# Kernel optimization log

Hardware: AMD Instinct MI355X
Metric: run time of the kernel (lower is better)

## Reference

```python
import jax, jax.numpy as jnp
import numpy as np

B, C, H, W = 16, 512, 64, 64
CB, CG = 64, 256  # bottleneck = C/8, g = C/2


def _conv1x1(x, w, b):
    # x: [B,Cin,H,W], w: [Cout,Cin] -> [B,Cout,H,W]
    return jnp.einsum('bchw,oc->bohw', x, w) + b[None, :, None, None]


def _avg_pool2(x):
    # 2x2 average pool, stride 2. x: [B,C,H,W] with even H,W.
    b, c, h, w = x.shape
    return x.reshape(b, c, h // 2, 2, w // 2, 2).mean(axis=(3, 5))


def setup_inputs() -> dict:
    key = jax.random.key(0)
    ks = jax.random.split(key, 6)
    s = 0.02
    return {
        'x': jax.random.normal(ks[0], (B, C, H, W), jnp.float32),
        'w_theta': jax.random.normal(ks[1], (CB, C), jnp.float32) * s,
        'b_theta': jnp.zeros((CB,), jnp.float32),
        'w_phi': jax.random.normal(ks[2], (CB, C), jnp.float32) * s,
        'b_phi': jnp.zeros((CB,), jnp.float32),
        'w_g': jax.random.normal(ks[3], (CG, C), jnp.float32) * s,
        'b_g': jnp.zeros((CG,), jnp.float32),
        'w_out': jax.random.normal(ks[4], (C, CG), jnp.float32) * s,
        'b_out': jnp.zeros((C,), jnp.float32),
        'gamma': jnp.zeros((1,), jnp.float32),
    }


def reference(x, w_theta, b_theta, w_phi, b_phi, w_g, b_g, w_out, b_out, gamma):
    b, c, h, w = x.shape
    n = h * w          # query locations
    m = n // 4         # pooled key/value locations

    theta = _conv1x1(x, w_theta, b_theta).reshape(b, CB, n)           # [B,CB,N]
    phi = _avg_pool2(_conv1x1(x, w_phi, b_phi)).reshape(b, CB, m)     # [B,CB,M]
    g = _avg_pool2(_conv1x1(x, w_g, b_g)).reshape(b, CG, m)           # [B,CG,M]

    logits = jnp.einsum('bcn,bcm->bnm', theta, phi)                   # [B,N,M]
    attn = jax.nn.softmax(logits, axis=-1)
    out = jnp.einsum('bcm,bnm->bcn', g, attn).reshape(b, CG, h, w)    # [B,CG,H,W]
    out = _conv1x1(out, w_out, b_out)                                 # [B,C,H,W]
    return gamma[0] * out + x
```

## Files before the change

### kernel.cpp

```cpp
#include <hip/hip_runtime.h>
#include <math.h>


typedef unsigned short u16;
typedef short bf16x8 __attribute__((ext_vector_type(8)));
typedef float f32x16 __attribute__((ext_vector_type(16)));
typedef u16 u16x4 __attribute__((ext_vector_type(4)));
typedef int i32x4 __attribute__((ext_vector_type(4)));

#define MFMA32 __builtin_amdgcn_mfma_f32_32x32x16_bf16
#define B_ 16
#define C_ 512
#define N_ 4096
#define M_ 1024
#define LOG2E 1.44269504088896f
#define FIXMAX 8.0f

__device__ __forceinline__ u16 f2b(float f) {
  unsigned u = __float_as_uint(f);
  return (u16)((u + 0x7FFFu + ((u >> 16) & 1u)) >> 16);
}
__device__ __forceinline__ unsigned cvtpk(float a, float b) {
  unsigned r;
  asm("v_cvt_pk_bf16_f32 %0, %1, %2" : "=v"(r) : "v"(a), "v"(b));
  return r;
}
__device__ __forceinline__ void permswap(unsigned &a, unsigned &b) {
  asm("v_permlane32_swap_b32 %0, %1" : "+v"(a), "+v"(b));
}
__device__ __forceinline__ float exp2v(float a) {
  float r;
  asm("v_exp_f32 %0, %1" : "=v"(r) : "v"(a));
  return r;
}
__device__ __forceinline__ void async_cp16(u16* lds, const u16* g) {
  __builtin_amdgcn_global_load_lds(
      (const __attribute__((address_space(1))) unsigned int*)g,
      (__attribute__((address_space(3))) unsigned int*)lds, 16, 0, 0);
}
__device__ __forceinline__ f32x16 fz16() {
  f32x16 z;
#pragma unroll
  for (int i = 0; i < 16; ++i) z[i] = 0.0f;
  return z;
}


__global__ __launch_bounds__(256) void cvt_all_kernel(
    const float* __restrict__ w_theta, const float* __restrict__ w_phi,
    const float* __restrict__ w_g, const float* __restrict__ w_out,
    const float* __restrict__ gamma, u16* __restrict__ dth, u16* __restrict__ dph,
    u16* __restrict__ dg, u16* __restrict__ dwo) {
  int i = blockIdx.x * 256 + threadIdx.x;
  if (i < 16384) {
    const float* s = (i < 8192) ? w_theta : w_phi;
    u16* d = (i < 8192) ? dth : dph;
    float scale = (i < 8192) ? LOG2E : 1.0f;
    int j = i & 8191;
    int o = j >> 7, c = (j & 127) * 4;
    float4 vv = *(const float4*)(s + (size_t)o * 512 + c);
    int idx = (((o >> 5) * 8 + (c >> 6)) * 4 + ((c >> 4) & 3)) * 512 +
              (((c >> 3) & 1) * 32 + (o & 31)) * 8 + (c & 7);
    u16x4 ot = {f2b(vv.x * scale), f2b(vv.y * scale), f2b(vv.z * scale), f2b(vv.w * scale)};
    *(u16x4*)(d + idx) = ot;
  } else if (i < 49152) {
    int j = i - 16384;
    int o = j >> 7, c = (j & 127) * 4;
    float4 vv = *(const float4*)(w_g + (size_t)o * 512 + c);
    int idx = (((o >> 5) * 8 + (c >> 6)) * 4 + ((c >> 4) & 3)) * 512 +
              (((c >> 3) & 1) * 32 + (o & 31)) * 8 + (c & 7);
    u16x4 ot = {f2b(vv.x), f2b(vv.y), f2b(vv.z), f2b(vv.w)};
    *(u16x4*)(dg + idx) = ot;
  } else {
    int j = i - 49152;
    int o = j >> 6, k = (j & 63) * 4;
    float scale = gamma[0];
    float4 vv = *(const float4*)(w_out + (size_t)o * 256 + k);
    int idx = ((o >> 5) * 16 + (k >> 4)) * 512 +
              (((k >> 3) & 1) * 32 + (o & 31)) * 8 + (k & 7);
    u16x4 ot = {f2b(vv.x * scale), f2b(vv.y * scale), f2b(vv.z * scale), f2b(vv.w * scale)};
    *(u16x4*)(dwo + idx) = ot;
  }
}

__global__ __launch_bounds__(512) void prep_kernel(
    const float* __restrict__ x, const u16* __restrict__ wth,
    const u16* __restrict__ wph, const u16* __restrict__ wg,
    const float* __restrict__ bth, const float* __restrict__ bph,
    const float* __restrict__ bg, u16* __restrict__ th, u16* __restrict__ ph,
    u16* __restrict__ vt) {
  __shared__ u16 xb[128 * 68];
  __shared__ u16 xpt[32 * 68];
  const int t = threadIdx.x;
  const int w = t >> 6, l = t & 63, lo = l & 31, hi = l >> 5;
  const int nb = blockIdx.x, b = blockIdx.y;
  const int n0 = nb * 128;
  const int lcol = (t & 31) * 4;
  const int lrow = t >> 5;

  f32x16 acc0 = fz16(), acc1 = fz16(), a_ph = fz16();

  float v[16];
  auto loadv = [&](int c0) {
#pragma unroll
    for (int i = 0; i < 4; ++i) {
      float4 f = *(const float4*)(x + ((size_t)(b * C_ + c0 + lrow + 16 * i)) * N_ + n0 + lcol);
      v[4*i] = f.x; v[4*i+1] = f.y; v[4*i+2] = f.z; v[4*i+3] = f.w;
    }
  };
  auto writeT = [&]() {
#pragma unroll
    for (int i = 0; i < 4; ++i) {
      int c = lrow + 16 * i;
      int blk = c >> 3;
#pragma unroll
      for (int k = 0; k < 4; ++k) {
        int n = lcol + k;
        int swz = ((n >> 2) ^ (n >> 5)) & 7;
        xb[n * 68 + ((blk ^ swz) * 8) + (c & 7)] = f2b(v[4*i+k]);
      }
    }
    float pA[4], pB[4];
#pragma unroll
    for (int i = 0; i < 4; ++i) {
      pA[i] = v[4*i] + v[4*i+1];
      pB[i] = v[4*i+2] + v[4*i+3];
    }
#pragma unroll
    for (int i = 0; i < 4; ++i) {
      pA[i] += __shfl_xor(pA[i], 16, 64);
      pB[i] += __shfl_xor(pB[i], 16, 64);
    }
    if ((t & 31) < 16) {
      int m0 = (t & 31) * 2;
#pragma unroll
      for (int i = 0; i < 4; ++i) {
        int c = lrow + 16 * i;
        xpt[m0 * 68 + c] = f2b(0.25f * pA[i]);
        xpt[(m0 + 1) * 68 + c] = f2b(0.25f * pB[i]);
      }
    }
  };
  auto domfma = [&](int c0b) {
    if (w < 4) {
      const int n = 32 * w + lo;
      const int rbase = n * 68;
      const int nswz = ((n >> 2) ^ (n >> 5)) & 7;
#pragma unroll
      for (int kh = 0; kh < 4; ++kh) {
        bf16x8 xa = *(const bf16x8*)(&xb[rbase + (((2*kh + hi) ^ nswz) * 8)]);
        bf16x8 w0 = *(const bf16x8*)(wth + ((c0b) * 4 + kh) * 512 + l * 8);
        bf16x8 w1 = *(const bf16x8*)(wth + ((8 + c0b) * 4 + kh) * 512 + l * 8);
        acc0 = MFMA32(xa, w0, acc0, 0, 0, 0);
        acc1 = MFMA32(xa, w1, acc1, 0, 0, 0);
      }
    } else {
      const int wg4 = w - 4;
      const u16* xpw = &xpt[lo * 68];
#pragma unroll
      for (int kh = 0; kh < 4; ++kh) {
        bf16x8 xp8 = *(const bf16x8*)(xpw + kh * 16 + hi * 8);
        bf16x8 g0 = *(const bf16x8*)(wg + ((16*wg4 + c0b) * 4 + kh) * 512 + l * 8);
        bf16x8 g1 = *(const bf16x8*)(wg + ((16*wg4 + 8 + c0b) * 4 + kh) * 512 + l * 8);
        acc0 = MFMA32(g0, xp8, acc0, 0, 0, 0);
        acc1 = MFMA32(g1, xp8, acc1, 0, 0, 0);
        if (wg4 < 2) {
          bf16x8 wp8 = *(const bf16x8*)(wph + ((wg4*8 + c0b) * 4 + kh) * 512 + l * 8);
          a_ph = MFMA32(xp8, wp8, a_ph, 0, 0, 0);
        }
      }
    }
  };

  loadv(0);
  for (int i = 0; i < 8; ++i) {
    if (i) __syncthreads();
    writeT();
    if (i < 7) loadv((i + 1) * 64);
    __syncthreads();
    domfma(i);
  }

  int rr[16];
#pragma unroll
  for (int r = 0; r < 16; ++r) rr[r] = (r & 3) + 8 * (r >> 2) + 4 * hi;

  if (w < 4) {
    u16* thb = th + (size_t)b * 262144;
#pragma unroll
    for (int r = 0; r < 16; ++r) {
      int sub = (((lo >> 3) & 1) * 32 + rr[r]) * 8 + (lo & 7);
      thb[((nb*4 + w)*4 + (lo >> 4)) * 512 + sub]     = f2b(acc0[r] + LOG2E * bth[lo]);
      thb[((nb*4 + w)*4 + 2 + (lo >> 4)) * 512 + sub] = f2b(acc1[r] + LOG2E * bth[32 + lo]);
    }
  } else {
    const int wg4 = w - 4;
    u16* vtb = vt + (size_t)b * 262144;
#pragma unroll
    for (int r = 0; r < 16; ++r) {
      int cg0 = 64 * wg4 + rr[r];
      int sub = (((lo >> 3) & 1) * 32 + rr[r]) * 8 + (lo & 7);
      int kk = (nb & 1) * 2 + (lo >> 4);
      vtb[(((nb >> 1) * 8 + 2*wg4) * 4 + kk) * 512 + sub]     = f2b(acc0[r] + bg[cg0]);
      vtb[(((nb >> 1) * 8 + 2*wg4 + 1) * 4 + kk) * 512 + sub] = f2b(acc1[r] + bg[cg0 + 32]);
    }
    if (wg4 < 2) {
      u16* phb = ph + (size_t)b * 65536;
#pragma unroll
      for (int r = 0; r < 16; ++r) {
        int sub = (((lo >> 3) & 1) * 32 + rr[r]) * 8 + (lo & 7);
        phb[(nb*4 + 2*wg4 + (lo >> 4)) * 512 + sub] = f2b(a_ph[r] + bph[32*wg4 + lo]);
      }
    }
  }
}

__global__ __launch_bounds__(512, 2) void attn_core_kernel(
    const u16* __restrict__ th, const u16* __restrict__ ph,
    const u16* __restrict__ vt, u16* __restrict__ Og) {
  __shared__ u16 smem[49152];

  const int t = threadIdx.x;
  const int w = t >> 6, l = t & 63;
  const int p = w & 3, h = w >> 2;
  const int flat = blockIdx.y * 16 + blockIdx.x;
  const int nf = (flat & 7) * 32 + (flat >> 3);
  const int b = nf >> 4, nb6 = nf & 15;
  const int jA = nb6 * 8 + p * 2, jB = jA + 1;

  const u16* thb = th + (size_t)b * 262144;
  const u16* phb = ph + (size_t)b * 65536;
  const u16* vtb = vt + (size_t)b * 262144;

  bf16x8 thA[4], thBt[4];
#pragma unroll
  for (int kh = 0; kh < 4; ++kh) {
    thA[kh]  = *(const bf16x8*)(thb + (jA * 4 + kh) * 512 + l * 8);
    thBt[kh] = *(const bf16x8*)(thb + (jB * 4 + kh) * 512 + l * 8);
  }

  f32x16 accA[4], accB[4];
#pragma unroll
  for (int ct = 0; ct < 4; ++ct) { accA[ct] = fz16(); accB[ct] = fz16(); }
  float spA[4] = {0.f, 0.f, 0.f, 0.f}, spB[4] = {0.f, 0.f, 0.f, 0.f};

  auto stage = [&](int k) {
    const int ic = k >> 1, jml2 = (k & 1) * 2;
    u16* base = &smem[(k & 3) * 10240];
#pragma unroll
    for (int i = 0; i < 2; ++i) {
      const int r = w + 8 * i;
      const u16* src = vtb + (size_t)((ic * 8 + (r >> 1)) * 4 + jml2 + (r & 1)) * 512 + l * 8;
      async_cp16(base + r * 512 + l * 8, src);
    }
    {
      const int o2 = (t & 255) * 8;
      async_cp16(base + 8192 + o2, phb + (size_t)k * 2048 + o2);
    }
  };

  auto packPf = [&](f32x16& S, bf16x8* Pf) {
#pragma unroll
    for (int s = 0; s < 2; ++s) {
      unsigned a0 = cvtpk(S[8*s+0], S[8*s+1]);
      unsigned a1 = cvtpk(S[8*s+2], S[8*s+3]);
      unsigned a2 = cvtpk(S[8*s+4], S[8*s+5]);
      unsigned a3 = cvtpk(S[8*s+6], S[8*s+7]);
      permswap(a0, a2);
      permswap(a1, a3);
      i32x4 wv = {(int)a0, (int)a1, (int)a2, (int)a3};
      Pf[s] = __builtin_bit_cast(bf16x8, wv);
    }
  };

  stage(0);
  stage(1);
  asm volatile("s_waitcnt vmcnt(3)" ::: "memory");
  __builtin_amdgcn_sched_barrier(0);
  __builtin_amdgcn_s_barrier();

  for (int k = 0; k < 32; ++k) {
    if (k < 30) stage(k + 2);

    const u16* Vs = &smem[(k & 3) * 10240];
    const u16* Ps = Vs + 8192;

    bf16x8 pf[4];
#pragma unroll
    for (int kh = 0; kh < 4; ++kh)
      pf[kh] = *(const bf16x8*)(Ps + kh * 512 + l * 8);

    f32x16 S = fz16();
#pragma unroll
    for (int kh = 0; kh < 4; ++kh) S = MFMA32(pf[kh], thA[kh], S, 0, 0, 0);
#pragma unroll
    for (int i = 0; i < 16; ++i) {
      S[i] = exp2v(S[i] - FIXMAX);
      spA[i & 3] += S[i];
    }
    bf16x8 PfA[2];
    packPf(S, PfA);

    f32x16 S2 = fz16();
#pragma unroll
    for (int kh = 0; kh < 4; ++kh) S2 = MFMA32(pf[kh], thBt[kh], S2, 0, 0, 0);
#pragma unroll
    for (int i = 0; i < 16; ++i) {
      S2[i] = exp2v(S2[i] - FIXMAX);
      spB[i & 3] += S2[i];
    }
    bf16x8 PfB[2];
    packPf(S2, PfB);

    __builtin_amdgcn_s_setprio(1);
#pragma unroll
    for (int ct2 = 0; ct2 < 4; ++ct2) {
      const u16* vp = Vs + (4 * h + ct2) * 1024 + l * 8;
      bf16x8 vf0 = *(const bf16x8*)(vp);
      bf16x8 vf1 = *(const bf16x8*)(vp + 512);
      accA[ct2] = MFMA32(vf0, PfA[0], accA[ct2], 0, 0, 0);
      accA[ct2] = MFMA32(vf1, PfA[1], accA[ct2], 0, 0, 0);
      accB[ct2] = MFMA32(vf0, PfB[0], accB[ct2], 0, 0, 0);
      accB[ct2] = MFMA32(vf1, PfB[1], accB[ct2], 0, 0, 0);
    }
    __builtin_amdgcn_s_setprio(0);

    if (k < 30) {
      asm volatile("s_waitcnt vmcnt(3)" ::: "memory");
      __builtin_amdgcn_sched_barrier(0);
      __builtin_amdgcn_s_barrier();
    } else if (k == 30) {
      asm volatile("s_waitcnt vmcnt(0)" ::: "memory");
      __builtin_amdgcn_sched_barrier(0);
      __builtin_amdgcn_s_barrier();
    }
  }

  float lA = (spA[0] + spA[1]) + (spA[2] + spA[3]);
  lA += __shfl_xor(lA, 32, 64);
  const float liA = 1.0f / lA;
  float lB = (spB[0] + spB[1]) + (spB[2] + spB[3]);
  lB += __shfl_xor(lB, 32, 64);
  const float liB = 1.0f / lB;

  auto packO = [&](f32x16* acc, float li, int jq) {
    u16* Ob = Og + (size_t)b * 1048576 + (size_t)jq * 16 * 512;
#pragma unroll
    for (int ct2 = 0; ct2 < 4; ++ct2) {
      f32x16& A = acc[ct2];
#pragma unroll
      for (int s = 0; s < 2; ++s) {
        unsigned a0 = cvtpk(A[8*s+0]*li, A[8*s+1]*li);
        unsigned a1 = cvtpk(A[8*s+2]*li, A[8*s+3]*li);
        unsigned a2 = cvtpk(A[8*s+4]*li, A[8*s+5]*li);
        unsigned a3 = cvtpk(A[8*s+6]*li, A[8*s+7]*li);
        permswap(a0, a2);
        permswap(a1, a3);
        i32x4 wv = {(int)a0, (int)a1, (int)a2, (int)a3};
        int f = 8 * h + 2 * ct2 + s;
        *(bf16x8*)(Ob + f * 512 + l * 8) = __builtin_bit_cast(bf16x8, wv);
      }
    }
  };
  packO(accA, liA, jA);
  packO(accB, liB, jB);
}

__global__ __launch_bounds__(512, 4) void outconv_kernel(
    const u16* __restrict__ Og, const u16* __restrict__ wo,
    const float* __restrict__ b_out, const float* __restrict__ gamma,
    const float* __restrict__ x, float* __restrict__ out) {
  const int t = threadIdx.x;
  const int w = t >> 6, l = t & 63, lo = l & 31, hi = l >> 5;
  const int p = w & 3, h = w >> 2;
  const int flat = blockIdx.y * 32 + blockIdx.x;
  const int nf = (flat & 7) * 64 + (flat >> 3);
  const int b = nf >> 5, nb5 = nf & 31;
  const int jqt = nb5 * 4 + p;
  const int qp = jqt * 32;

  const u16* Ob = Og + (size_t)b * 1048576 + (size_t)jqt * 16 * 512;
  bf16x8 Of[16];
#pragma unroll
  for (int f = 0; f < 16; ++f)
    Of[f] = *(const bf16x8*)(Ob + f * 512 + l * 8);

  int rr[16];
#pragma unroll
  for (int r = 0; r < 16; ++r) rr[r] = (r & 3) + 8 * (r >> 2) + 4 * hi;

  const float gamma0 = gamma[0];
  for (int ctc = 0; ctc < 8; ++ctc) {
    f32x16 facc = fz16();
    const u16* wp = wo + (size_t)((8 * h + ctc) * 16) * 512 + l * 8;
#pragma unroll
    for (int f = 0; f < 16; ++f) {
      bf16x8 wfr = *(const bf16x8*)(wp + f * 512);
      facc = MFMA32(wfr, Of[f], facc, 0, 0, 0);
    }
#pragma unroll
    for (int r = 0; r < 16; ++r) {
      int c = 256 * h + 32 * ctc + rr[r];
      size_t idx = ((size_t)(b * C_ + c)) * N_ + qp + lo;
      float xv = __builtin_nontemporal_load(&x[idx]);
      __builtin_nontemporal_store(facc[r] + gamma0 * b_out[c] + xv, &out[idx]);
    }
  }
}

extern "C" void kernel_launch(void* const* d_in, const int* in_sizes, int n_in,
                              void* d_out, int out_size, void* d_ws, size_t ws_size,
                              hipStream_t stream) {
  (void)in_sizes; (void)n_in; (void)out_size; (void)ws_size;
  const float* x       = (const float*)d_in[0];
  const float* w_theta = (const float*)d_in[1];
  const float* b_theta = (const float*)d_in[2];
  const float* w_phi   = (const float*)d_in[3];
  const float* b_phi   = (const float*)d_in[4];
  const float* w_g     = (const float*)d_in[5];
  const float* b_g     = (const float*)d_in[6];
  const float* w_out   = (const float*)d_in[7];
  const float* b_out   = (const float*)d_in[8];
  const float* gamma   = (const float*)d_in[9];
  float* out = (float*)d_out;

  char* ws = (char*)d_ws;
  u16* th  = (u16*)(ws);
  u16* ph  = (u16*)(ws + 8388608);
  u16* vt  = (u16*)(ws + 10485760);
  u16* wth = (u16*)(ws + 18874368);
  u16* wph = (u16*)(ws + 18939904);
  u16* wg  = (u16*)(ws + 19005440);
  u16* wo  = (u16*)(ws + 19267584);
  u16* Og  = (u16*)(ws + 19529728);

  cvt_all_kernel<<<320, 256, 0, stream>>>(w_theta, w_phi, w_g, w_out, gamma,
                                          wth, wph, wg, wo);
  prep_kernel<<<dim3(32, 16), 512, 0, stream>>>(x, wth, wph, wg, b_theta, b_phi,
                                                b_g, th, ph, vt);
  attn_core_kernel<<<dim3(16, 16), 512, 0, stream>>>(th, ph, vt, Og);
  outconv_kernel<<<dim3(32, 16), 512, 0, stream>>>(Og, wo, b_out, gamma, x, out);
}
```

Measured before the change: 165.1 us.

## Deepen attention core LDS pipeline to six buffers processing two stages per barrier

```diff
diff --git a/kernel.cpp b/kernel.cpp
--- a/kernel.cpp
+++ b/kernel.cpp
@@ -218,7 +218,7 @@
 __global__ __launch_bounds__(512, 2) void attn_core_kernel(
     const u16* __restrict__ th, const u16* __restrict__ ph,
     const u16* __restrict__ vt, u16* __restrict__ Og) {
-  __shared__ u16 smem[49152];
+  __shared__ u16 smem[61440];
 
   const int t = threadIdx.x;
   const int w = t >> 6, l = t & 63;
@@ -244,9 +244,9 @@
   for (int ct = 0; ct < 4; ++ct) { accA[ct] = fz16(); accB[ct] = fz16(); }
   float spA[4] = {0.f, 0.f, 0.f, 0.f}, spB[4] = {0.f, 0.f, 0.f, 0.f};
 
-  auto stage = [&](int k) {
+  auto stage = [&](int k, int buf) {
     const int ic = k >> 1, jml2 = (k & 1) * 2;
-    u16* base = &smem[(k & 3) * 10240];
+    u16* base = &smem[buf * 10240];
 #pragma unroll
     for (int i = 0; i < 2; ++i) {
       const int r = w + 8 * i;
@@ -273,16 +273,8 @@
     }
   };
 
-  stage(0);
-  stage(1);
-  asm volatile("s_waitcnt vmcnt(3)" ::: "memory");
-  __builtin_amdgcn_sched_barrier(0);
-  __builtin_amdgcn_s_barrier();
-
-  for (int k = 0; k < 32; ++k) {
-    if (k < 30) stage(k + 2);
-
-    const u16* Vs = &smem[(k & 3) * 10240];
+  auto process = [&](int buf) {
+    const u16* Vs = &smem[buf * 10240];
     const u16* Ps = Vs + 8192;
 
     bf16x8 pf[4];
@@ -324,16 +316,39 @@
       accB[ct2] = MFMA32(vf1, PfB[1], accB[ct2], 0, 0, 0);
     }
     __builtin_amdgcn_s_setprio(0);
-
-    if (k < 30) {
-      asm volatile("s_waitcnt vmcnt(3)" ::: "memory");
+  };
+
+  stage(0, 0);
+  stage(1, 1);
+  stage(2, 2);
+  stage(3, 3);
+  asm volatile("s_waitcnt vmcnt(6)" ::: "memory");
+  __builtin_amdgcn_sched_barrier(0);
+  __builtin_amdgcn_s_barrier();
+
+  int bc = 0;
+  for (int wnd = 0; wnd < 16; ++wnd) {
+    const int k0 = 2 * wnd;
+    if (k0 + 4 < 32) {
+      int bs = bc + 4; if (bs >= 6) bs -= 6;
+      int bs2 = bs + 1; if (bs2 >= 6) bs2 -= 6;
+      stage(k0 + 4, bs);
+      stage(k0 + 5, bs2);
+    }
+    int bc2 = bc + 1; if (bc2 >= 6) bc2 -= 6;
+    process(bc);
+    process(bc2);
+
+    if (wnd < 14) {
+      asm volatile("s_waitcnt vmcnt(6)" ::: "memory");
       __builtin_amdgcn_sched_barrier(0);
       __builtin_amdgcn_s_barrier();
-    } else if (k == 30) {
+    } else if (wnd == 14) {
       asm volatile("s_waitcnt vmcnt(0)" ::: "memory");
       __builtin_amdgcn_sched_barrier(0);
       __builtin_amdgcn_s_barrier();
     }
+    bc = bc2 + 1; if (bc >= 6) bc -= 6;
   }
 
   float lA = (spA[0] + spA[1]) + (spA[2] + spA[3]);
```

New measurement: 184.3 us. 1.12x slower.
